# Optimization experiments

Measured on AMD Instinct MI355X. Metric: run time of the kernel, lower is better.

## Reference

```python
import jax, jax.numpy as jnp
from jax import lax
import numpy as np

B, H, W, C = 8, 32, 32, 256
SOFTMAX_SCALE = 10.0
DN = ('NHWC', 'HWIO', 'NHWC')


def _patches(t):
    # t: [b,h,w,c] -> [b,h,w,3,3,c], SAME zero padding, stride 1 (tf.image.extract_patches)
    b, h, w, c = t.shape
    tp = jnp.pad(t, ((0, 0), (1, 1), (1, 1), (0, 0)))
    cols = [tp[:, i:i + h, j:j + w, :] for i in range(3) for j in range(3)]
    return jnp.stack(cols, axis=3).reshape(b, h, w, 3, 3, c)


def _diag_fuse(z):
    # conv2d of [L,L] map with eye(3) kernel, SAME padding:
    # out[i,j] = z[i-1,j-1] + z[i,j] + z[i+1,j+1] (zero padded)
    dr = jnp.pad(z, ((1, 0), (1, 0)))[:-1, :-1]
    ul = jnp.pad(z, ((0, 1), (0, 1)))[1:, 1:]
    return z + dr + ul


def _conv(x, w):
    return lax.conv_general_dilated(x, w, (1, 1), 'SAME', dimension_numbers=DN)


def _attend(xi, wi, mmean):
    # xi: [h,w,c]; wi: [3,3,c,L] patch kernels; mmean: [L] mean of mask patches
    h, w, c = xi.shape
    L = h * w
    norm = jnp.maximum(jnp.sqrt(jnp.sum(wi * wi, axis=(0, 1, 2))), 1e-4)
    yi = _conv(xi[None], wi / norm)[0]  # [h,w,L] cosine-sim scores
    # fuse: diagonal propagation along both spatial orderings
    z = yi.reshape(L, L)
    z = _diag_fuse(z).reshape(h, w, h, w).transpose(1, 0, 3, 2).reshape(L, L)
    z = _diag_fuse(z).reshape(w, h, w, h).transpose(1, 0, 3, 2)  # [h,w,h,w]
    yi = z.reshape(h, w, L)
    mm = (mmean == 1.0).astype(yi.dtype)  # valid-patch mask per location
    yi = jax.nn.softmax(yi * mm * SOFTMAX_SCALE, axis=-1) * mm
    # conv2d_transpose(yi, wi, stride 1, SAME) == conv with hw-flipped kernel,
    # in/out channels swapped (TF filter layout [h,w,out=C,in=L])
    k2 = jnp.flip(wi, (0, 1)).transpose(0, 1, 3, 2)  # [3,3,L,C]
    return _conv(yi[None], k2)[0]  # [h,w,c]


def _forward(x, mask, conv_w, conv_b, conv1_w, conv1_b, conv2_w, conv2_b):
    b, h, w, c = x.shape
    L = h * w
    # rate=1: tf.image.resize to same size is identity, f == b == x
    wi = _patches(x).reshape(b, L, 3, 3, c).transpose(0, 2, 3, 4, 1)  # [b,3,3,c,L]
    mmean = _patches(mask).mean(axis=(3, 4, 5)).reshape(b, L)
    y = jax.vmap(_attend)(x, wi, mmean)  # [b,h,w,c]
    ycat = jnp.concatenate([y, x], axis=-1)  # [b,h,w,2c]
    g1 = jax.nn.sigmoid(_conv(ycat, conv1_w) + conv1_b)
    g2 = jax.nn.sigmoid(_conv(ycat, conv2_w) + conv2_b)
    gate = (g1 + g2) * 0.5
    out = gate * (_conv(ycat, conv_w) + conv_b)
    return out, jnp.ones_like(mask)


def setup_inputs() -> dict:
    key = jax.random.key(0)
    ks = jax.random.split(key, 4)
    x = jax.random.normal(ks[0], (B, H, W, C), jnp.float32)
    mask = jnp.ones((B, H, W, 1), jnp.float32)
    conv_w = jax.random.normal(ks[1], (3, 3, 2 * C, C), jnp.float32) * 0.02
    conv_b = jnp.zeros((C,), jnp.float32)
    conv1_w = jax.random.normal(ks[2], (1, 1, 2 * C, C), jnp.float32) * 0.02
    conv1_b = jnp.zeros((C,), jnp.float32)
    conv2_w = jax.random.normal(ks[3], (3, 3, 2 * C, C), jnp.float32) * 0.02
    conv2_b = jnp.zeros((C,), jnp.float32)
    return {'x': x, 'mask': mask, 'conv_w': conv_w, 'conv_b': conv_b,
            'conv1_w': conv1_w, 'conv1_b': conv1_b, 'conv2_w': conv2_w, 'conv2_b': conv2_b}


def reference(x, mask, conv_w, conv_b, conv1_w, conv1_b, conv2_w, conv2_b):
    return _forward(x, mask, conv_w, conv_b, conv1_w, conv1_b, conv2_w, conv2_b)
```

## Files before the change

### kernel.cpp

```cpp
#include <hip/hip_runtime.h>
#include <math.h>

typedef unsigned short u16;
typedef __bf16 bf16x8 __attribute__((ext_vector_type(8)));
typedef float f32x4 __attribute__((ext_vector_type(4)));

#define NPOS 1156
#define GSTR 1160
#define GOFF (GSTR * 1156)
#define YSTR 1032
#define YOFF (YSTR * 1026)
#define POS34(p) ((((p) >> 5) + 1) * 34 + ((p) & 31) + 1)

__device__ __constant__ const int kDiagOff[9] = {
    -35 * (GSTR + 1), -34 * (GSTR + 1), -33 * (GSTR + 1),
    -1 * (GSTR + 1),  0,                1 * (GSTR + 1),
    33 * (GSTR + 1),  34 * (GSTR + 1),  35 * (GSTR + 1)};

__device__ __forceinline__ u16 f2bf(float f) {
  unsigned int u = __builtin_bit_cast(unsigned int, f);
  return (u16)((u + 0x7FFFu + ((u >> 16) & 1u)) >> 16);
}
__device__ __forceinline__ float bf2f(u16 v) {
  unsigned int u = ((unsigned int)v) << 16;
  return __builtin_bit_cast(float, u);
}
__device__ __forceinline__ void gload16(const void* g, void* l) {
  __builtin_amdgcn_global_load_lds(
      (const __attribute__((address_space(1))) void*)g,
      (__attribute__((address_space(3))) void*)l, 16, 0, 0);
}
__device__ __forceinline__ int posOf(int p) { return POS34(p); }

__global__ __launch_bounds__(256) void cast_x(
    const float* __restrict__ x, u16* __restrict__ xpad, u16* __restrict__ xT) {
  int blk = blockIdx.x;
  int b = blk >> 5, h = blk & 31;
  __shared__ u16 T[256][33];
  const float* xrow = x + ((size_t)b * 1024 + h * 32) * 256;
  int tid = threadIdx.x;
  for (int idx = tid; idx < 8192; idx += 256) {
    int w = idx >> 8, c = idx & 255;
    u16 v = f2bf(xrow[(size_t)w * 256 + c]);
    T[c][w] = v;
    xpad[((size_t)b * NPOS + (h + 1) * 34 + (w + 1)) * 256 + c] = v;
  }
  __syncthreads();
  int c = tid;
  unsigned int* dp = (unsigned int*)(xT + ((size_t)(b * 256 + c)) * 1024 + h * 32);
  const unsigned int* sp = (const unsigned int*)&T[c][0];
#pragma unroll
  for (int u = 0; u < 16; ++u) dp[u] = sp[u];
}

__global__ __launch_bounds__(256) void wtrans(
    const float* __restrict__ src, u16* __restrict__ dst, int K) {
  int k0 = blockIdx.x * 32;
  __shared__ u16 T[256][34];
  int tid = threadIdx.x;
  for (int idx = tid; idx < 8192; idx += 256) {
    int kr = idx >> 8, c = idx & 255;
    T[c][kr] = f2bf(src[(size_t)(k0 + kr) * 256 + c]);
  }
  __syncthreads();
  int c = tid;
  unsigned int* dp = (unsigned int*)(dst + (size_t)c * K + k0);
  const unsigned int* sp = (const unsigned int*)&T[c][0];
#pragma unroll
  for (int u = 0; u < 16; ++u) dp[u] = sp[u];
}

__global__ __launch_bounds__(256) void gram_base(
    const u16* __restrict__ xpad, float* __restrict__ Gpad) {
  const int b = blockIdx.z;
  const int m0 = blockIdx.x << 7;
  const int n0 = blockIdx.y << 7;
  const u16* xb = xpad + (size_t)b * NPOS * 256;
  __shared__ __align__(16) u16 As[128 * 64];
  __shared__ __align__(16) u16 Bs[128 * 64];
  const int tid = threadIdx.x;
  const int lane = tid & 63;
  const int wave = tid >> 6;
  const int wm = wave >> 1, wn = wave & 1;
  const int srow = lane >> 3;
  const int cswz = ((lane & 7) ^ srow) << 3;
  int pa[4], pb[4];
#pragma unroll
  for (int i = 0; i < 4; ++i) {
    pa[i] = posOf(m0 + wave * 32 + i * 8 + srow);
    pb[i] = posOf(n0 + wave * 32 + i * 8 + srow);
  }
  int aidx[4][2], bidx[4][2];
#pragma unroll
  for (int f = 0; f < 4; ++f)
#pragma unroll
    for (int ks = 0; ks < 2; ++ks) {
      int ra = wm * 64 + f * 16 + (lane & 15);
      int rb = wn * 64 + f * 16 + (lane & 15);
      int k16 = ks * 4 + (lane >> 4);
      aidx[f][ks] = ra * 64 + ((k16 ^ (ra & 7)) << 3);
      bidx[f][ks] = rb * 64 + ((k16 ^ (rb & 7)) << 3);
    }
  f32x4 acc[4][4] = {};
  for (int c0 = 0; c0 < 256; c0 += 64) {
    __syncthreads();
#pragma unroll
    for (int i = 0; i < 4; ++i) {
      gload16(xb + (size_t)pa[i] * 256 + c0 + cswz, &As[(wave * 32 + i * 8) * 64]);
      gload16(xb + (size_t)pb[i] * 256 + c0 + cswz, &Bs[(wave * 32 + i * 8) * 64]);
    }
    __syncthreads();
#pragma unroll
    for (int ks = 0; ks < 2; ++ks) {
      bf16x8 a[4], bb[4];
#pragma unroll
      for (int f = 0; f < 4; ++f) a[f] = *(const bf16x8*)(As + aidx[f][ks]);
#pragma unroll
      for (int f = 0; f < 4; ++f) bb[f] = *(const bf16x8*)(Bs + bidx[f][ks]);
#pragma unroll
      for (int mi = 0; mi < 4; ++mi)
#pragma unroll
        for (int ni = 0; ni < 4; ++ni)
          acc[mi][ni] = __builtin_amdgcn_mfma_f32_16x16x32_bf16(a[mi], bb[ni], acc[mi][ni], 0, 0, 0);
    }
  }
  float* Gb = Gpad + (size_t)b * GOFF;
  const int r0 = (lane >> 4) << 2;
  const int cb0 = n0 + wn * 64 + (lane & 15);
#pragma unroll
  for (int mi = 0; mi < 4; ++mi) {
    int row = m0 + wm * 64 + mi * 16 + r0;
    int rp = POS34(row);
#pragma unroll
    for (int ni = 0; ni < 4; ++ni) {
      int cp = POS34(cb0 + ni * 16);
#pragma unroll
      for (int r = 0; r < 4; ++r)
        Gb[(size_t)(rp + r) * GSTR + cp] = acc[mi][ni][r];
    }
  }
}

__global__ __launch_bounds__(256) void norm_mm(
    const float* __restrict__ Gpad, const float* __restrict__ mask,
    float* __restrict__ invn, float* __restrict__ mm, float* __restrict__ ones_out) {
  int idx = blockIdx.x * 256 + threadIdx.x;
  int b = idx >> 10, l = idx & 1023;
  const float* Gb = Gpad + (size_t)b * GOFF;
  size_t dbase = (size_t)POS34(l) * (GSTR + 1);
  float d = 0.f;
#pragma unroll
  for (int t = 0; t < 9; ++t) d += Gb[dbase + kDiagOff[t]];
  invn[idx] = 1.0f / fmaxf(sqrtf(d), 1e-4f);
  int lh = l >> 5, lw = l & 31;
  float s = 0.f;
  for (int dh = -1; dh <= 1; ++dh)
    for (int dw = -1; dw <= 1; ++dw) {
      int hh = lh + dh, wv = lw + dw;
      if (hh >= 0 && hh < 32 && wv >= 0 && wv < 32) s += mask[b * 1024 + hh * 32 + wv];
    }
  mm[idx] = ((s / 9.0f) == 1.0f) ? 1.0f : 0.0f;
  ones_out[idx] = 1.0f;
}

__global__ __launch_bounds__(256) void patch_norm_p(
    const float* __restrict__ Gpad, const float* __restrict__ invn,
    u16* __restrict__ Ylin) {
  const int b = blockIdx.y;
  const int p0 = blockIdx.x << 2;
  const float* Gb = Gpad + (size_t)b * GOFF;
  u16* Yb = Ylin + (size_t)b * YOFF;
  const int tid = threadIdx.x;
  const int l0 = tid << 2;
  const int lp0 = POS34(l0);
  const float4 iv = *(const float4*)(invn + (b << 10) + l0);
#pragma unroll
  for (int r = 0; r < 4; ++r) {
    int p = p0 + r;
    int base = POS34(p) * GSTR + lp0;
    float v[9][4];
#pragma unroll
    for (int t = 0; t < 9; ++t) {
      const float* q = Gb + (base + kDiagOff[t]);
      v[t][0] = q[0]; v[t][1] = q[1]; v[t][2] = q[2]; v[t][3] = q[3];
    }
    float s0 = 0.f, s1 = 0.f, s2 = 0.f, s3 = 0.f;
#pragma unroll
    for (int t = 0; t < 9; ++t) { s0 += v[t][0]; s1 += v[t][1]; s2 += v[t][2]; s3 += v[t][3]; }
    u16* yw = Yb + (size_t)(p + 1) * YSTR + l0 + 1;
    yw[0] = f2bf(s0 * iv.x); yw[1] = f2bf(s1 * iv.y);
    yw[2] = f2bf(s2 * iv.z); yw[3] = f2bf(s3 * iv.w);
  }
}

__device__ __forceinline__ float z1p(const u16* __restrict__ Yb, int r, int c) {
  size_t a = (size_t)(r + 1) * YSTR + (c + 1);
  return bf2f(Yb[a]) + bf2f(Yb[a - (YSTR + 1)]) + bf2f(Yb[a + (YSTR + 1)]);
}

__global__ __launch_bounds__(256) void fuse_softmax(
    const u16* __restrict__ Ylin, const float* __restrict__ mm,
    u16* __restrict__ Apad2) {
  const int bi = blockIdx.x;
  const int b = bi >> 10, i = bi & 1023;
  const u16* Yb = Ylin + (size_t)b * YOFF;
  __shared__ float smm[1024];
  __shared__ float red[256];
  const int tid = threadIdx.x;
  for (int t = tid; t < 1024; t += 256) smm[t] = mm[(b << 10) + t];
  __syncthreads();
  const int si = ((i & 31) << 5) | (i >> 5);
  const int rm = (si >= 1) ? ((((si - 1) & 31) << 5) | ((si - 1) >> 5)) : -1;
  const int rp = (si <= 1022) ? ((((si + 1) & 31) << 5) | ((si + 1) >> 5)) : -1;
  float logit[4];
  float lmax = -3.0e38f;
#pragma unroll
  for (int q = 0; q < 4; ++q) {
    int j = tid + (q << 8);
    int sj = ((j & 31) << 5) | (j >> 5);
    float S = z1p(Yb, i, j);
    if (rm >= 0 && sj >= 1) {
      int col = (((sj - 1) & 31) << 5) | ((sj - 1) >> 5);
      S += z1p(Yb, rm, col);
    }
    if (rp >= 0 && sj <= 1022) {
      int col = (((sj + 1) & 31) << 5) | ((sj + 1) >> 5);
      S += z1p(Yb, rp, col);
    }
    float lg = S * smm[j] * 10.0f;
    logit[q] = lg;
    lmax = fmaxf(lmax, lg);
  }
  red[tid] = lmax; __syncthreads();
  for (int off = 128; off > 0; off >>= 1) {
    if (tid < off) red[tid] = fmaxf(red[tid], red[tid + off]);
    __syncthreads();
  }
  float M = red[0];
  __syncthreads();
  float ex[4];
  float lsum = 0.f;
#pragma unroll
  for (int q = 0; q < 4; ++q) { ex[q] = expf(logit[q] - M); lsum += ex[q]; }
  red[tid] = lsum; __syncthreads();
  for (int off = 128; off > 0; off >>= 1) {
    if (tid < off) red[tid] += red[tid + off];
    __syncthreads();
  }
  float inv = 1.0f / red[0];
  u16* Ap = Apad2 + (size_t)b * GOFF + (size_t)POS34(i) * GSTR;
#pragma unroll
  for (int q = 0; q < 4; ++q) {
    int j = tid + (q << 8);
    Ap[POS34(j)] = f2bf(smm[j] * ex[q] * inv);
  }
}

__global__ __launch_bounds__(256) void afuse_p(
    const u16* __restrict__ Apad2, u16* __restrict__ Afuse) {
  const int b = blockIdx.y;
  const int q0 = blockIdx.x << 2;
  const u16* Ab = Apad2 + (size_t)b * GOFF;
  u16* Fb = Afuse + ((size_t)b << 20);
  const int tid = threadIdx.x;
  const int l0 = tid << 2;
  const int lp0 = POS34(l0);
#pragma unroll
  for (int r = 0; r < 4; ++r) {
    int q = q0 + r;
    int base = POS34(q) * GSTR + lp0;
    float v[9][4];
#pragma unroll
    for (int t = 0; t < 9; ++t) {
      const u16* p = Ab + (base - kDiagOff[t]);
      v[t][0] = bf2f(p[0]); v[t][1] = bf2f(p[1]);
      v[t][2] = bf2f(p[2]); v[t][3] = bf2f(p[3]);
    }
    float s0 = 0.f, s1 = 0.f, s2 = 0.f, s3 = 0.f;
#pragma unroll
    for (int t = 0; t < 9; ++t) { s0 += v[t][0]; s1 += v[t][1]; s2 += v[t][2]; s3 += v[t][3]; }
    u16* fw = Fb + (size_t)q * 1024 + l0;
    fw[0] = f2bf(s0); fw[1] = f2bf(s1); fw[2] = f2bf(s2); fw[3] = f2bf(s3);
  }
}

__global__ __launch_bounds__(256) void paste_gemm(
    const u16* __restrict__ Afuse, const u16* __restrict__ xT, u16* __restrict__ ypad) {
  const int bm0 = blockIdx.x << 6;
  const int b = bm0 >> 10;
  const int q0 = bm0 & 1023;
  const int n0 = blockIdx.y << 6;
  const u16* Ab = Afuse + ((size_t)b << 20);
  const u16* xTb = xT + ((size_t)b << 18);
  __shared__ __align__(16) u16 As[2][64 * 64];
  __shared__ __align__(16) u16 Bs[2][64 * 64];
  const int tid = threadIdx.x;
  const int lane = tid & 63;
  const int wave = tid >> 6;
  const int wm = wave >> 1, wn = wave & 1;
  const int srow = lane >> 3;
  const int cswz = ((lane & 7) ^ srow) << 3;
  int aidx[2][2], bidx[2][2];
#pragma unroll
  for (int ks = 0; ks < 2; ++ks) {
    int k16 = ks * 4 + (lane >> 4);
#pragma unroll
    for (int f = 0; f < 2; ++f) {
      int ra = wm * 32 + f * 16 + (lane & 15);
      aidx[f][ks] = ra * 64 + ((k16 ^ (ra & 7)) << 3);
      int rb = wn * 32 + f * 16 + (lane & 15);
      bidx[f][ks] = rb * 64 + ((k16 ^ (rb & 7)) << 3);
    }
  }
  auto STAGE = [&](int kt, int pb) {
    int l0 = kt << 6;
#pragma unroll
    for (int i = 0; i < 2; ++i) {
      int ar = wave * 16 + i * 8 + srow;
      gload16(Ab + (size_t)(q0 + ar) * 1024 + l0 + cswz, &As[pb][ar * 64]);
      gload16(xTb + (size_t)(n0 + ar) * 1024 + l0 + cswz, &Bs[pb][ar * 64]);
    }
  };
  f32x4 acc[2][2] = {};
  STAGE(0, 0);
  __syncthreads();
  for (int kt = 0; kt < 16; ++kt) {
    int pb = kt & 1;
    if (kt < 15) STAGE(kt + 1, pb ^ 1);
#pragma unroll
    for (int ks = 0; ks < 2; ++ks) {
      bf16x8 a[2], bb[2];
#pragma unroll
      for (int f = 0; f < 2; ++f) a[f] = *(const bf16x8*)(&As[pb][0] + aidx[f][ks]);
#pragma unroll
      for (int f = 0; f < 2; ++f) bb[f] = *(const bf16x8*)(&Bs[pb][0] + bidx[f][ks]);
#pragma unroll
      for (int mi = 0; mi < 2; ++mi)
#pragma unroll
        for (int ni = 0; ni < 2; ++ni)
          acc[mi][ni] = __builtin_amdgcn_mfma_f32_16x16x32_bf16(a[mi], bb[ni], acc[mi][ni], 0, 0, 0);
    }
    __syncthreads();
  }
  u16* yb = ypad + (size_t)b * NPOS * 256;
  const int r0 = (lane >> 4) << 2;
#pragma unroll
  for (int mi = 0; mi < 2; ++mi) {
    int qb = q0 + wm * 32 + mi * 16 + r0;
#pragma unroll
    for (int ni = 0; ni < 2; ++ni) {
      int c = n0 + wn * 32 + ni * 16 + (lane & 15);
#pragma unroll
      for (int r = 0; r < 4; ++r)
        yb[(size_t)posOf(qb + r) * 256 + c] = f2bf(acc[mi][ni][r]);
    }
  }
}

__global__ __launch_bounds__(256) void final_fused(
    const u16* __restrict__ ypad, const u16* __restrict__ xpad,
    const u16* __restrict__ w0T, const u16* __restrict__ w1T,
    const u16* __restrict__ w2T,
    const float* __restrict__ b0, const float* __restrict__ b1,
    const float* __restrict__ b2, float* __restrict__ out) {
  const int m0 = blockIdx.x << 6;
  const int b = m0 >> 10;
  const int q0 = m0 & 1023;
  const int n0 = blockIdx.y << 6;
  const u16* yb = ypad + (size_t)b * NPOS * 256;
  const u16* xb = xpad + (size_t)b * NPOS * 256;
  __shared__ __align__(16) u16 As[2][64 * 64];
  __shared__ __align__(16) u16 B0s[2][64 * 64];
  __shared__ __align__(16) u16 B1s[2][64 * 64];
  __shared__ __align__(16) u16 B2s[2][64 * 64];
  const int tid = threadIdx.x;
  const int lane = tid & 63;
  const int wave = tid >> 6;
  const int wm = wave >> 1, wn = wave & 1;
  const int srow = lane >> 3;
  const int cswz = ((lane & 7) ^ srow) << 3;
  int posA[2];
#pragma unroll
  for (int i = 0; i < 2; ++i) posA[i] = posOf(q0 + wave * 16 + i * 8 + srow);
  int aidx[2][2], bidx[2][2];
#pragma unroll
  for (int ks = 0; ks < 2; ++ks) {
    int k16 = ks * 4 + (lane >> 4);
#pragma unroll
    for (int f = 0; f < 2; ++f) {
      int ra = wm * 32 + f * 16 + (lane & 15);
      aidx[f][ks] = ra * 64 + ((k16 ^ (ra & 7)) << 3);
      int rb = wn * 32 + f * 16 + (lane & 15);
      bidx[f][ks] = rb * 64 + ((k16 ^ (rb & 7)) << 3);
    }
  }
  auto STAGE = [&](int kt, int pb) {
    int s = kt >> 3;
    int c0k = (kt & 7) << 6;
    const u16* basep = (c0k < 256) ? yb : xb;
    int coff = c0k & 255;
    int dpos = (s / 3 - 1) * 34 + (s % 3 - 1);
#pragma unroll
    for (int i = 0; i < 2; ++i) {
      int ar = wave * 16 + i * 8 + srow;
      gload16(basep + (size_t)(posA[i] + dpos) * 256 + coff + cswz, &As[pb][ar * 64]);
      size_t krow = (size_t)(n0 + ar) * 4608 + s * 512 + c0k + cswz;
      gload16(w0T + krow, &B0s[pb][ar * 64]);
      gload16(w2T + krow, &B2s[pb][ar * 64]);
      if (s == 4)
        gload16(w1T + (size_t)(n0 + ar) * 512 + c0k + cswz, &B1s[pb][ar * 64]);
    }
  };
  f32x4 acc0[2][2] = {}, acc1[2][2] = {}, acc2[2][2] = {};
  STAGE(0, 0);
  __syncthreads();
  for (int kt = 0; kt < 72; ++kt) {
    const int pb = kt & 1;
    if (kt < 71) STAGE(kt + 1, pb ^ 1);
    const int s = kt >> 3;
#pragma unroll
    for (int ks = 0; ks < 2; ++ks) {
      bf16x8 a[2], v0[2], v2[2];
#pragma unroll
      for (int f = 0; f < 2; ++f) a[f] = *(const bf16x8*)(&As[pb][0] + aidx[f][ks]);
#pragma unroll
      for (int f = 0; f < 2; ++f) v0[f] = *(const bf16x8*)(&B0s[pb][0] + bidx[f][ks]);
#pragma unroll
      for (int f = 0; f < 2; ++f) v2[f] = *(const bf16x8*)(&B2s[pb][0] + bidx[f][ks]);
#pragma unroll
      for (int mi = 0; mi < 2; ++mi)
#pragma unroll
        for (int ni = 0; ni < 2; ++ni) {
          acc0[mi][ni] = __builtin_amdgcn_mfma_f32_16x16x32_bf16(a[mi], v0[ni], acc0[mi][ni], 0, 0, 0);
          acc2[mi][ni] = __builtin_amdgcn_mfma_f32_16x16x32_bf16(a[mi], v2[ni], acc2[mi][ni], 0, 0, 0);
        }
      if (s == 4) {
        bf16x8 v1[2];
#pragma unroll
        for (int f = 0; f < 2; ++f) v1[f] = *(const bf16x8*)(&B1s[pb][0] + bidx[f][ks]);
#pragma unroll
        for (int mi = 0; mi < 2; ++mi)
#pragma unroll
          for (int ni = 0; ni < 2; ++ni)
            acc1[mi][ni] = __builtin_amdgcn_mfma_f32_16x16x32_bf16(a[mi], v1[ni], acc1[mi][ni], 0, 0, 0);
      }
    }
    __syncthreads();
  }
  const int r0 = (lane >> 4) << 2;
#pragma unroll
  for (int ni = 0; ni < 2; ++ni) {
    int co = n0 + wn * 32 + ni * 16 + (lane & 15);
    float q0b = b0[co], q1b = b1[co], q2b = b2[co];
#pragma unroll
    for (int mi = 0; mi < 2; ++mi) {
      int m = m0 + wm * 32 + mi * 16 + r0;
#pragma unroll
      for (int r = 0; r < 4; ++r) {
        float g1 = 1.f / (1.f + expf(-(acc1[mi][ni][r] + q1b)));
        float g2 = 1.f / (1.f + expf(-(acc2[mi][ni][r] + q2b)));
        out[(size_t)(m + r) * 256 + co] = 0.5f * (g1 + g2) * (acc0[mi][ni][r] + q0b);
      }
    }
  }
}


extern "C" void kernel_launch(void* const* d_in, const int* in_sizes, int n_in,
                              void* d_out, int out_size, void* d_ws, size_t ws_size,
                              hipStream_t stream) {
  const float* x = (const float*)d_in[0];
  const float* mask = (const float*)d_in[1];
  const float* conv_w = (const float*)d_in[2];
  const float* conv_b = (const float*)d_in[3];
  const float* conv1_w = (const float*)d_in[4];
  const float* conv1_b = (const float*)d_in[5];
  const float* conv2_w = (const float*)d_in[6];
  const float* conv2_b = (const float*)d_in[7];
  float* out = (float*)d_out;
  char* wsb = (char*)d_ws;

  float* Gpad  = (float*)(wsb + 0);
  u16* Apad2   = (u16*)(wsb + 0);
  u16* Ylin    = (u16*)(wsb + 42910720);
  u16* Afuse   = (u16*)(wsb + 42910720);
  u16* xpad    = (u16*)(wsb + 59852032);
  u16* ypad    = (u16*)(wsb + 64587008);
  u16* xT      = (u16*)(wsb + 69321984);
  u16* w0T     = (u16*)(wsb + 73516288);
  u16* w2T     = (u16*)(wsb + 75875584);
  u16* w1T     = (u16*)(wsb + 78234880);
  float* invn  = (float*)(wsb + 78497024);
  float* mmb   = (float*)(wsb + 78529792);

  hipMemsetAsync(wsb, 0, 69321984, stream);

  cast_x<<<256, 256, 0, stream>>>(x, xpad, xT);
  wtrans<<<144, 256, 0, stream>>>(conv_w, w0T, 4608);
  wtrans<<<144, 256, 0, stream>>>(conv2_w, w2T, 4608);
  wtrans<<<16, 256, 0, stream>>>(conv1_w, w1T, 512);

  gram_base<<<dim3(8, 8, 8), 256, 0, stream>>>(xpad, Gpad);
  norm_mm<<<32, 256, 0, stream>>>(Gpad, mask, invn, mmb, out + 2097152);
  patch_norm_p<<<dim3(256, 8), 256, 0, stream>>>(Gpad, invn, Ylin);
  hipMemsetAsync(wsb, 0, 21455360, stream);
  fuse_softmax<<<8192, 256, 0, stream>>>(Ylin, mmb, Apad2);
  afuse_p<<<dim3(256, 8), 256, 0, stream>>>(Apad2, Afuse);
  paste_gemm<<<dim3(128, 4), 256, 0, stream>>>(Afuse, xT, ypad);
  final_fused<<<dim3(128, 4), 256, 0, stream>>>(ypad, xpad, w0T, w1T, w2T,
                                                conv_b, conv1_b, conv2_b, out);
}
```

Measured before the change: 281.8 us.

## Replace bulk memsets with border-only zeroing and split final conv into separate GEMMs

```diff
diff --git a/kernel.cpp b/kernel.cpp
--- a/kernel.cpp
+++ b/kernel.cpp
@@ -31,6 +31,63 @@
       (__attribute__((address_space(3))) void*)l, 16, 0, 0);
 }
 __device__ __forceinline__ int posOf(int p) { return POS34(p); }
+
+__global__ __launch_bounds__(256) void zb_pre(
+    float* __restrict__ Gpad, u16* __restrict__ Ylin,
+    u16* __restrict__ xpad, u16* __restrict__ ypad) {
+  int bi = blockIdx.x, tid = threadIdx.x;
+  if (bi < 9248) {
+    int b = bi / 1156, r = bi - b * 1156;
+    float* row = Gpad + (size_t)b * GOFF + (size_t)r * GSTR;
+    int rm = r % 34;
+    bool brow = (r < 34) || (r >= 1122) || (rm == 0) || (rm == 33);
+    if (brow) {
+      for (int c = tid; c < GSTR; c += 256) row[c] = 0.f;
+    } else {
+      for (int c = tid; c < GSTR; c += 256) {
+        int cm = c % 34;
+        if (c < 34 || c >= 1122 || cm == 0 || cm == 33) row[c] = 0.f;
+      }
+    }
+    return;
+  }
+  bi -= 9248;
+  if (bi < 8208) {
+    int b = bi / 1026, r = bi - b * 1026;
+    u16* row = Ylin + (size_t)b * YOFF + (size_t)r * YSTR;
+    if (r == 0 || r == 1025) {
+      for (int c = tid; c < YSTR; c += 256) row[c] = 0;
+    } else if (tid < 8) {
+      row[tid == 0 ? 0 : 1024 + tid] = 0;
+    }
+    return;
+  }
+  bi -= 8208;
+  int arr = bi / 9248;
+  bi -= arr * 9248;
+  int b = bi / 1156, p = bi - b * 1156;
+  int pm = p % 34;
+  bool bp = (p < 34) || (p >= 1122) || (pm == 0) || (pm == 33);
+  if (!bp) return;
+  u16* dst = (arr ? ypad : xpad) + ((size_t)b * NPOS + p) * 256;
+  dst[tid] = 0;
+}
+
+__global__ __launch_bounds__(256) void zb_apad(u16* __restrict__ Apad2) {
+  int bi = blockIdx.x, tid = threadIdx.x;
+  int b = bi / 1156, r = bi - b * 1156;
+  u16* row = Apad2 + (size_t)b * GOFF + (size_t)r * GSTR;
+  int rm = r % 34;
+  bool brow = (r < 34) || (r >= 1122) || (rm == 0) || (rm == 33);
+  if (brow) {
+    for (int c = tid; c < GSTR; c += 256) row[c] = 0;
+  } else {
+    for (int c = tid; c < GSTR; c += 256) {
+      int cm = c % 34;
+      if (c < 34 || c >= 1122 || cm == 0 || cm == 33) row[c] = 0;
+    }
+  }
+}
 
 __global__ __launch_bounds__(256) void cast_x(
     const float* __restrict__ x, u16* __restrict__ xpad, u16* __restrict__ xT) {
@@ -292,8 +349,8 @@
   const int n0 = blockIdx.y << 6;
   const u16* Ab = Afuse + ((size_t)b << 20);
   const u16* xTb = xT + ((size_t)b << 18);
-  __shared__ __align__(16) u16 As[2][64 * 64];
-  __shared__ __align__(16) u16 Bs[2][64 * 64];
+  __shared__ __align__(16) u16 As[64 * 64];
+  __shared__ __align__(16) u16 Bs[64 * 64];
   const int tid = threadIdx.x;
   const int lane = tid & 63;
   const int wave = tid >> 6;
@@ -312,35 +369,29 @@
       bidx[f][ks] = rb * 64 + ((k16 ^ (rb & 7)) << 3);
     }
   }
-  auto STAGE = [&](int kt, int pb) {
-    int l0 = kt << 6;
+  f32x4 acc[2][2] = {};
+  for (int l0 = 0; l0 < 1024; l0 += 64) {
+    __syncthreads();
 #pragma unroll
     for (int i = 0; i < 2; ++i) {
       int ar = wave * 16 + i * 8 + srow;
-      gload16(Ab + (size_t)(q0 + ar) * 1024 + l0 + cswz, &As[pb][ar * 64]);
-      gload16(xTb + (size_t)(n0 + ar) * 1024 + l0 + cswz, &Bs[pb][ar * 64]);
-    }
-  };
-  f32x4 acc[2][2] = {};
-  STAGE(0, 0);
-  __syncthreads();
-  for (int kt = 0; kt < 16; ++kt) {
-    int pb = kt & 1;
-    if (kt < 15) STAGE(kt + 1, pb ^ 1);
+      gload16(Ab + (size_t)(q0 + ar) * 1024 + l0 + cswz, &As[ar * 64]);
+      gload16(xTb + (size_t)(n0 + ar) * 1024 + l0 + cswz, &Bs[ar * 64]);
+    }
+    __syncthreads();
 #pragma unroll
     for (int ks = 0; ks < 2; ++ks) {
       bf16x8 a[2], bb[2];
 #pragma unroll
-      for (int f = 0; f < 2; ++f) a[f] = *(const bf16x8*)(&As[pb][0] + aidx[f][ks]);
-#pragma unroll
-      for (int f = 0; f < 2; ++f) bb[f] = *(const bf16x8*)(&Bs[pb][0] + bidx[f][ks]);
+      for (int f = 0; f < 2; ++f) a[f] = *(const bf16x8*)(As + aidx[f][ks]);
+#pragma unroll
+      for (int f = 0; f < 2; ++f) bb[f] = *(const bf16x8*)(Bs + bidx[f][ks]);
 #pragma unroll
       for (int mi = 0; mi < 2; ++mi)
 #pragma unroll
         for (int ni = 0; ni < 2; ++ni)
           acc[mi][ni] = __builtin_amdgcn_mfma_f32_16x16x32_bf16(a[mi], bb[ni], acc[mi][ni], 0, 0, 0);
     }
-    __syncthreads();
   }
   u16* yb = ypad + (size_t)b * NPOS * 256;
   const int r0 = (lane >> 4) << 2;
@@ -357,22 +408,21 @@
   }
 }
 
-__global__ __launch_bounds__(256) void final_fused(
+__global__ __launch_bounds__(256) void conv_split(
     const u16* __restrict__ ypad, const u16* __restrict__ xpad,
-    const u16* __restrict__ w0T, const u16* __restrict__ w1T,
-    const u16* __restrict__ w2T,
-    const float* __restrict__ b0, const float* __restrict__ b1,
-    const float* __restrict__ b2, float* __restrict__ out) {
+    const u16* __restrict__ w0T, const u16* __restrict__ w2T,
+    float* __restrict__ c0buf, float* __restrict__ c2buf) {
   const int m0 = blockIdx.x << 6;
   const int b = m0 >> 10;
   const int q0 = m0 & 1023;
-  const int n0 = blockIdx.y << 6;
+  const int sel = blockIdx.y >> 2;
+  const int n0 = (blockIdx.y & 3) << 6;
+  const u16* wT = sel ? w2T : w0T;
+  float* dst = sel ? c2buf : c0buf;
   const u16* yb = ypad + (size_t)b * NPOS * 256;
   const u16* xb = xpad + (size_t)b * NPOS * 256;
-  __shared__ __align__(16) u16 As[2][64 * 64];
-  __shared__ __align__(16) u16 B0s[2][64 * 64];
-  __shared__ __align__(16) u16 B1s[2][64 * 64];
-  __shared__ __align__(16) u16 B2s[2][64 * 64];
+  __shared__ __align__(16) u16 As[64 * 64];
+  __shared__ __align__(16) u16 Bs[64 * 64];
   const int tid = threadIdx.x;
   const int lane = tid & 63;
   const int wave = tid >> 6;
@@ -382,6 +432,10 @@
   int posA[2];
 #pragma unroll
   for (int i = 0; i < 2; ++i) posA[i] = posOf(q0 + wave * 16 + i * 8 + srow);
+  const u16* wrow[2];
+#pragma unroll
+  for (int i = 0; i < 2; ++i)
+    wrow[i] = wT + (size_t)(n0 + wave * 16 + i * 8 + srow) * 4608 + cswz;
   int aidx[2][2], bidx[2][2];
 #pragma unroll
   for (int ks = 0; ks < 2; ++ks) {
@@ -394,75 +448,147 @@
       bidx[f][ks] = rb * 64 + ((k16 ^ (rb & 7)) << 3);
     }
   }
-  auto STAGE = [&](int kt, int pb) {
-    int s = kt >> 3;
-    int c0k = (kt & 7) << 6;
+  f32x4 acc[2][2] = {};
+  for (int kt = 0; kt < 72; ++kt) {
+    const int s = kt >> 3;
+    const int c0k = (kt & 7) << 6;
     const u16* basep = (c0k < 256) ? yb : xb;
-    int coff = c0k & 255;
-    int dpos = (s / 3 - 1) * 34 + (s % 3 - 1);
+    const int coff = c0k & 255;
+    const int dpos = (s / 3 - 1) * 34 + (s % 3 - 1);
+    __syncthreads();
 #pragma unroll
     for (int i = 0; i < 2; ++i) {
       int ar = wave * 16 + i * 8 + srow;
-      gload16(basep + (size_t)(posA[i] + dpos) * 256 + coff + cswz, &As[pb][ar * 64]);
-      size_t krow = (size_t)(n0 + ar) * 4608 + s * 512 + c0k + cswz;
-      gload16(w0T + krow, &B0s[pb][ar * 64]);
-      gload16(w2T + krow, &B2s[pb][ar * 64]);
-      if (s == 4)
-        gload16(w1T + (size_t)(n0 + ar) * 512 + c0k + cswz, &B1s[pb][ar * 64]);
-    }
-  };
-  f32x4 acc0[2][2] = {}, acc1[2][2] = {}, acc2[2][2] = {};
-  STAGE(0, 0);
-  __syncthreads();
-  for (int kt = 0; kt < 72; ++kt) {
-    const int pb = kt & 1;
-    if (kt < 71) STAGE(kt + 1, pb ^ 1);
-    const int s = kt >> 3;
+      gload16(basep + (size_t)(posA[i] + dpos) * 256 + coff + cswz, &As[ar * 64]);
+      gload16(wrow[i] + (kt << 6), &Bs[ar * 64]);
+    }
+    __syncthreads();
 #pragma unroll
     for (int ks = 0; ks < 2; ++ks) {
-      bf16x8 a[2], v0[2], v2[2];
-#pragma unroll
-      for (int f = 0; f < 2; ++f) a[f] = *(const bf16x8*)(&As[pb][0] + aidx[f][ks]);
-#pragma unroll
-      for (int f = 0; f < 2; ++f) v0[f] = *(const bf16x8*)(&B0s[pb][0] + bidx[f][ks]);
-#pragma unroll
-      for (int f = 0; f < 2; ++f) v2[f] = *(const bf16x8*)(&B2s[pb][0] + bidx[f][ks]);
+      bf16x8 a[2], bb[2];
+#pragma unroll
+      for (int f = 0; f < 2; ++f) a[f] = *(const bf16x8*)(As + aidx[f][ks]);
+#pragma unroll
+      for (int f = 0; f < 2; ++f) bb[f] = *(const bf16x8*)(Bs + bidx[f][ks]);
 #pragma unroll
       for (int mi = 0; mi < 2; ++mi)
 #pragma unroll
-        for (int ni = 0; ni < 2; ++ni) {
-          acc0[mi][ni] = __builtin_amdgcn_mfma_f32_16x16x32_bf16(a[mi], v0[ni], acc0[mi][ni], 0, 0, 0);
-          acc2[mi][ni] = __builtin_amdgcn_mfma_f32_16x16x32_bf16(a[mi], v2[ni], acc2[mi][ni], 0, 0, 0);
-        }
-      if (s == 4) {
-        bf16x8 v1[2];
-#pragma unroll
-        for (int f = 0; f < 2; ++f) v1[f] = *(const bf16x8*)(&B1s[pb][0] + bidx[f][ks]);
-#pragma unroll
-        for (int mi = 0; mi < 2; ++mi)
-#pragma unroll
-          for (int ni = 0; ni < 2; ++ni)
-            acc1[mi][ni] = __builtin_amdgcn_mfma_f32_16x16x32_bf16(a[mi], v1[ni], acc1[mi][ni], 0, 0, 0);
-      }
-    }
-    __syncthreads();
+        for (int ni = 0; ni < 2; ++ni)
+          acc[mi][ni] = __builtin_amdgcn_mfma_f32_16x16x32_bf16(a[mi], bb[ni], acc[mi][ni], 0, 0, 0);
+    }
   }
   const int r0 = (lane >> 4) << 2;
 #pragma unroll
-  for (int ni = 0; ni < 2; ++ni) {
-    int co = n0 + wn * 32 + ni * 16 + (lane & 15);
-    float q0b = b0[co], q1b = b1[co], q2b = b2[co];
-#pragma unroll
-    for (int mi = 0; mi < 2; ++mi) {
-      int m = m0 + wm * 32 + mi * 16 + r0;
-#pragma unroll
-      for (int r = 0; r < 4; ++r) {
-        float g1 = 1.f / (1.f + expf(-(acc1[mi][ni][r] + q1b)));
-        float g2 = 1.f / (1.f + expf(-(acc2[mi][ni][r] + q2b)));
-        out[(size_t)(m + r) * 256 + co] = 0.5f * (g1 + g2) * (acc0[mi][ni][r] + q0b);
-      }
-    }
-  }
+  for (int mi = 0; mi < 2; ++mi) {
+    int m = m0 + wm * 32 + mi * 16 + r0;
+#pragma unroll
+    for (int ni = 0; ni < 2; ++ni) {
+      int co = n0 + wn * 32 + ni * 16 + (lane & 15);
+#pragma unroll
+      for (int r = 0; r < 4; ++r)
+        dst[(size_t)(m + r) * 256 + co] = acc[mi][ni][r];
+    }
+  }
+}
+
+__global__ __launch_bounds__(256) void conv1_gemm(
+    const u16* __restrict__ ypad, const u16* __restrict__ xpad,
+    const u16* __restrict__ w1T, float* __restrict__ c1buf) {
+  const int m0 = blockIdx.x << 6;
+  const int b = m0 >> 10;
+  const int q0 = m0 & 1023;
+  const int n0 = blockIdx.y << 6;
+  const u16* yb = ypad + (size_t)b * NPOS * 256;
+  const u16* xb = xpad + (size_t)b * NPOS * 256;
+  __shared__ __align__(16) u16 As[64 * 64];
+  __shared__ __align__(16) u16 Bs[64 * 64];
+  const int tid = threadIdx.x;
+  const int lane = tid & 63;
+  const int wave = tid >> 6;
+  const int wm = wave >> 1, wn = wave & 1;
+  const int srow = lane >> 3;
+  const int cswz = ((lane & 7) ^ srow) << 3;
+  int posA[2];
+#pragma unroll
+  for (int i = 0; i < 2; ++i) posA[i] = posOf(q0 + wave * 16 + i * 8 + srow);
+  int aidx[2][2], bidx[2][2];
+#pragma unroll
+  for (int ks = 0; ks < 2; ++ks) {
+    int k16 = ks * 4 + (lane >> 4);
+#pragma unroll
+    for (int f = 0; f < 2; ++f) {
+      int ra = wm * 32 + f * 16 + (lane & 15);
+      aidx[f][ks] = ra * 64 + ((k16 ^ (ra & 7)) << 3);
+      int rb = wn * 32 + f * 16 + (lane & 15);
+      bidx[f][ks] = rb * 64 + ((k16 ^ (rb & 7)) << 3);
+    }
+  }
+  f32x4 acc[2][2] = {};
+  for (int kt = 0; kt < 8; ++kt) {
+    const int c0k = kt << 6;
+    const u16* basep = (c0k < 256) ? yb : xb;
+    const int coff = c0k & 255;
+    __syncthreads();
+#pragma unroll
+    for (int i = 0; i < 2; ++i) {
+      int ar = wave * 16 + i * 8 + srow;
+      gload16(basep + (size_t)posA[i] * 256 + coff + cswz, &As[ar * 64]);
+      gload16(w1T + (size_t)(n0 + ar) * 512 + c0k + cswz, &Bs[ar * 64]);
+    }
+    __syncthreads();
+#pragma unroll
+    for (int ks = 0; ks < 2; ++ks) {
+      bf16x8 a[2], bb[2];
+#pragma unroll
+      for (int f = 0; f < 2; ++f) a[f] = *(const bf16x8*)(As + aidx[f][ks]);
+#pragma unroll
+      for (int f = 0; f < 2; ++f) bb[f] = *(const bf16x8*)(Bs + bidx[f][ks]);
+#pragma unroll
+      for (int mi = 0; mi < 2; ++mi)
+#pragma unroll
+        for (int ni = 0; ni < 2; ++ni)
+          acc[mi][ni] = __builtin_amdgcn_mfma_f32_16x16x32_bf16(a[mi], bb[ni], acc[mi][ni], 0, 0, 0);
+    }
+  }
+  const int r0 = (lane >> 4) << 2;
+#pragma unroll
+  for (int mi = 0; mi < 2; ++mi) {
+    int m = m0 + wm * 32 + mi * 16 + r0;
+#pragma unroll
+    for (int ni = 0; ni < 2; ++ni) {
+      int co = n0 + wn * 32 + ni * 16 + (lane & 15);
+#pragma unroll
+      for (int r = 0; r < 4; ++r)
+        c1buf[(size_t)(m + r) * 256 + co] = acc[mi][ni][r];
+    }
+  }
+}
+
+__global__ __launch_bounds__(256) void gate_out(
+    const float* __restrict__ c0buf, const float* __restrict__ c1buf,
+    const float* __restrict__ c2buf, const float* __restrict__ b0,
+    const float* __restrict__ b1, const float* __restrict__ b2,
+    float* __restrict__ out) {
+  size_t i4 = ((size_t)blockIdx.x * 256 + threadIdx.x) * 4;
+  int co = (int)(i4 & 255);
+  float4 v0 = *(const float4*)(c0buf + i4);
+  float4 v1 = *(const float4*)(c1buf + i4);
+  float4 v2 = *(const float4*)(c2buf + i4);
+  float4 q0 = *(const float4*)(b0 + co);
+  float4 q1 = *(const float4*)(b1 + co);
+  float4 q2 = *(const float4*)(b2 + co);
+  float4 o;
+  const float* pv0 = (const float*)&v0; const float* pv1 = (const float*)&v1;
+  const float* pv2 = (const float*)&v2; const float* pq0 = (const float*)&q0;
+  const float* pq1 = (const float*)&q1; const float* pq2 = (const float*)&q2;
+  float* po = (float*)&o;
+#pragma unroll
+  for (int j = 0; j < 4; ++j) {
+    float g1 = 1.f / (1.f + expf(-(pv1[j] + pq1[j])));
+    float g2 = 1.f / (1.f + expf(-(pv2[j] + pq2[j])));
+    po[j] = 0.5f * (g1 + g2) * (pv0[j] + pq0[j]);
+  }
+  *(float4*)(out + i4) = o;
 }
 
 
@@ -482,6 +608,9 @@
 
   float* Gpad  = (float*)(wsb + 0);
   u16* Apad2   = (u16*)(wsb + 0);
+  float* c0buf = (float*)(wsb + 0);
+  float* c2buf = (float*)(wsb + 8388608);
+  float* c1buf = (float*)(wsb + 16777216);
   u16* Ylin    = (u16*)(wsb + 42910720);
   u16* Afuse   = (u16*)(wsb + 42910720);
   u16* xpad    = (u16*)(wsb + 59852032);
@@ -493,8 +622,7 @@
   float* invn  = (float*)(wsb + 78497024);
   float* mmb   = (float*)(wsb + 78529792);
 
-  hipMemsetAsync(wsb, 0, 69321984, stream);
-
+  zb_pre<<<35952, 256, 0, stream>>>(Gpad, Ylin, xpad, ypad);
   cast_x<<<256, 256, 0, stream>>>(x, xpad, xT);
   wtrans<<<144, 256, 0, stream>>>(conv_w, w0T, 4608);
   wtrans<<<144, 256, 0, stream>>>(conv2_w, w2T, 4608);
@@ -503,10 +631,11 @@
   gram_base<<<dim3(8, 8, 8), 256, 0, stream>>>(xpad, Gpad);
   norm_mm<<<32, 256, 0, stream>>>(Gpad, mask, invn, mmb, out + 2097152);
   patch_norm_p<<<dim3(256, 8), 256, 0, stream>>>(Gpad, invn, Ylin);
-  hipMemsetAsync(wsb, 0, 21455360, stream);
+  zb_apad<<<9248, 256, 0, stream>>>(Apad2);
   fuse_softmax<<<8192, 256, 0, stream>>>(Ylin, mmb, Apad2);
   afuse_p<<<dim3(256, 8), 256, 0, stream>>>(Apad2, Afuse);
   paste_gemm<<<dim3(128, 4), 256, 0, stream>>>(Afuse, xT, ypad);
-  final_fused<<<dim3(128, 4), 256, 0, stream>>>(ypad, xpad, w0T, w1T, w2T,
-                                                conv_b, conv1_b, conv2_b, out);
-}
+  conv1_gemm<<<dim3(128, 4), 256, 0, stream>>>(ypad, xpad, w1T, c1buf);
+  conv_split<<<dim3(128, 8), 256, 0, stream>>>(ypad, xpad, w0T, w2T, c0buf, c2buf);
+  gate_out<<<2048, 256, 0, stream>>>(c0buf, c1buf, c2buf, conv_b, conv1_b, conv2_b, out);
+}
```

Measured after the change: 281.4 us. Within noise of the previous version (-0.2%).
